# Performance work log

Measured on AMD Instinct MI355X. Metric: run time of the kernel, lower is better.

## Reference

```python
import jax, jax.numpy as jnp
import numpy as np

EMBED = 1024
HEADS = 16
HEAD_DIM = EMBED // HEADS


def setup_inputs() -> dict:
    key = jax.random.key(0)
    ks = jax.random.split(key, 8)
    N, L = 2, 2048
    s = 0.02
    return {
        "values": jax.random.normal(ks[0], (N, L, EMBED), jnp.float32),
        "keys": jax.random.normal(ks[1], (N, L, EMBED), jnp.float32),
        "queries": jax.random.normal(ks[2], (N, L, EMBED), jnp.float32),
        # per-head projection weights, SHARED across heads (nn.Linear(head_dim, head_dim))
        "Wv": jax.random.normal(ks[3], (HEAD_DIM, HEAD_DIM), jnp.float32) * s,
        "Wk": jax.random.normal(ks[4], (HEAD_DIM, HEAD_DIM), jnp.float32) * s,
        "Wq": jax.random.normal(ks[5], (HEAD_DIM, HEAD_DIM), jnp.float32) * s,
        "Wo": jax.random.normal(ks[6], (EMBED, EMBED), jnp.float32) * s,
        "bo": jax.random.normal(ks[7], (EMBED,), jnp.float32) * s,
    }


def reference(values, keys, queries, Wv, Wk, Wq, Wo, bo):
    N, Lq, _ = queries.shape
    Lk = keys.shape[1]
    Lv = values.shape[1]
    # split heads: (N, L, H, D)
    v = values.reshape(N, Lv, HEADS, HEAD_DIM)
    k = keys.reshape(N, Lk, HEADS, HEAD_DIM)
    q = queries.reshape(N, Lq, HEADS, HEAD_DIM)
    # per-head linear (weight shared across heads); nn.Linear computes x @ W.T
    v = jnp.einsum('nlhd,ed->nlhe', v, Wv)
    k = jnp.einsum('nlhd,ed->nlhe', k, Wk)
    q = jnp.einsum('nlhd,ed->nlhe', q, Wq)
    # scores (N, H, Lq, Lk); NOTE: scale uses sqrt(embed_size), as in the original
    scores = jnp.einsum('nqhd,nkhd->nhqk', q, k) / jnp.sqrt(jnp.float32(EMBED))
    attn = jax.nn.softmax(scores, axis=-1)
    out = jnp.einsum('nhql,nlhd->nqhd', attn, v).reshape(N, Lq, EMBED)
    out = out @ Wo.T + bo
    return out
```

## Files before the change

### kernel.cpp

```cpp
#include <hip/hip_runtime.h>
#include <hip/hip_bf16.h>

#define EMBED 1024
#define HEADS 16
#define HD 64
#define NB 2
#define LSEQ 2048

typedef __bf16 bf16x8 __attribute__((ext_vector_type(8)));
typedef float f32x4 __attribute__((ext_vector_type(4)));

static __device__ __forceinline__ __bf16 f2b(float x) {
    union { __hip_bfloat16 h; __bf16 b; } u;
    u.h = __float2bfloat16(x);
    return u.b;
}
static __device__ __forceinline__ bf16x8 cvt8(float4 a, float4 b) {
    bf16x8 r;
    r[0] = f2b(a.x); r[1] = f2b(a.y); r[2] = f2b(a.z); r[3] = f2b(a.w);
    r[4] = f2b(b.x); r[5] = f2b(b.y); r[6] = f2b(b.z); r[7] = f2b(b.w);
    return r;
}
static __device__ __forceinline__ unsigned short b2u(float x) {
    union { __hip_bfloat16 h; unsigned short u; } c;
    c.h = __float2bfloat16(x);
    return c.u;
}

#define GLD16(g, l) __builtin_amdgcn_global_load_lds( \
    (const __attribute__((address_space(1))) void*)(g), \
    (__attribute__((address_space(3))) void*)(l), 16, 0, 0)


__global__ __launch_bounds__(256) void proj_kernel(
    const float* __restrict__ vals,
    const float* __restrict__ keys,
    const float* __restrict__ quer,
    const float* __restrict__ Wv,
    const float* __restrict__ Wk,
    const float* __restrict__ Wq,
    __hip_bfloat16* __restrict__ QF,
    __hip_bfloat16* __restrict__ KF,
    __hip_bfloat16* __restrict__ VF)
{
    int b      = blockIdx.x;
    int tensor = b % 3;
    int rem    = b / 3;
    int n      = rem >> 7;
    int lt     = (rem >> 2) & 31;
    int hg     = rem & 3;
    int t = threadIdx.x, w = t >> 6, lane = t & 63;
    int m16 = lane & 15, quad = lane >> 4;
    int l0 = lt * 64 + w * 16;

    const float* X = (tensor == 0) ? quer : (tensor == 1 ? keys : vals);
    const float* W = (tensor == 0) ? Wq   : (tensor == 1 ? Wk   : Wv);
    float scale = (tensor == 0) ? (1.44269504088896340736f / 32.0f) : 1.0f;

    bf16x8 wf[4][2];
#pragma unroll
    for (int f = 0; f < 4; ++f)
#pragma unroll
        for (int kk = 0; kk < 2; ++kk) {
            const float* wp = W + (f * 16 + m16) * HD + kk * 32 + quad * 8;
            wf[f][kk] = cvt8(*(const float4*)wp, *(const float4*)(wp + 4));
        }

#pragma unroll
    for (int hh = 0; hh < 4; ++hh) {
        int h = hg * 4 + hh;
        const float* xb = X + ((size_t)n * LSEQ + l0 + m16) * EMBED + h * HD + quad * 8;
        bf16x8 xf[2];
#pragma unroll
        for (int kk = 0; kk < 2; ++kk)
            xf[kk] = cvt8(*(const float4*)(xb + kk * 32), *(const float4*)(xb + kk * 32 + 4));

        size_t nhb = (size_t)(n * HEADS + h) * 131072;
        if (tensor != 2) {
            f32x4 acc[4] = {};
#pragma unroll
            for (int f = 0; f < 4; ++f) {
                acc[f] = __builtin_amdgcn_mfma_f32_16x16x32_bf16(wf[f][0], xf[0], acc[f], 0, 0, 0);
                acc[f] = __builtin_amdgcn_mfma_f32_16x16x32_bf16(wf[f][1], xf[1], acc[f], 0, 0, 0);
            }
            int key = l0 + m16;
#pragma unroll
            for (int f = 0; f < 4; ++f) {
                union { ushort4 u; unsigned short s[4]; } p;
#pragma unroll
                for (int r = 0; r < 4; ++r) p.s[r] = b2u(acc[f][r] * scale);
                int kk   = f >> 1;
                int qk2  = (f & 1) * 2 + (quad >> 1);
                int j4   = (quad & 1) * 4;
                __hip_bfloat16* dst;
                if (tensor == 0) {
                    dst = QF + nhb + (size_t)(l0 >> 4) * 1024 + kk * 512
                        + (qk2 * 16 + m16) * 8 + j4;
                } else {
                    dst = KF + nhb + (size_t)(key >> 5) * 2048
                        + ((key & 1) * 2 + kk) * 512
                        + (qk2 * 16 + ((key & 31) >> 1)) * 8 + j4;
                }
                *(ushort4*)dst = p.u;
            }
        } else {
            f32x4 acc[4] = {};
#pragma unroll
            for (int f = 0; f < 4; ++f) {
                acc[f] = __builtin_amdgcn_mfma_f32_16x16x32_bf16(xf[0], wf[f][0], acc[f], 0, 0, 0);
                acc[f] = __builtin_amdgcn_mfma_f32_16x16x32_bf16(xf[1], wf[f][1], acc[f], 0, 0, 0);
            }
            int keyq  = l0 + quad * 4;
            int c     = keyq >> 5;
            int quadv = (keyq & 31) >> 3;
            int j4    = (quad & 1) * 4;
#pragma unroll
            for (int f = 0; f < 4; ++f) {
                union { ushort4 u; unsigned short s[4]; } p;
#pragma unroll
                for (int r = 0; r < 4; ++r) p.s[r] = b2u(acc[f][r]);
                __hip_bfloat16* dst = VF + nhb + (size_t)c * 2048 + f * 512
                    + quadv * 128 + m16 * 8 + j4;
                *(ushort4*)dst = p.u;
            }
        }
    }
}

__global__ __launch_bounds__(256) void wcvt_kernel(
    const float* __restrict__ Wo, __hip_bfloat16* __restrict__ Wob)
{
    int base = (blockIdx.x * 256 + threadIdx.x) * 16;
#pragma unroll
    for (int j = 0; j < 16; j += 4) {
        float4 w4 = *(const float4*)(Wo + base + j);
        __hip_bfloat16 o[4] = {
            __float2bfloat16(w4.x), __float2bfloat16(w4.y),
            __float2bfloat16(w4.z), __float2bfloat16(w4.w)};
        *(ushort4*)(Wob + base + j) = *(const ushort4*)o;
    }
}

#define CHUNKS 32

#define LOADK(KFR, c_) do { \
    const __hip_bfloat16* kc_ = kp + (size_t)(c_) * 2048; \
    KFR[0][0] = *(const bf16x8*)(kc_); \
    KFR[0][1] = *(const bf16x8*)(kc_ + 512); \
    KFR[1][0] = *(const bf16x8*)(kc_ + 1024); \
    KFR[1][1] = *(const bf16x8*)(kc_ + 1536); \
} while (0)

#define LOADV(c_) do { \
    const __hip_bfloat16* vc_ = vp + (size_t)(c_) * 2048; \
    vf[0] = *(const bf16x8*)(vc_); \
    vf[1] = *(const bf16x8*)(vc_ + 512); \
    vf[2] = *(const bf16x8*)(vc_ + 1024); \
    vf[3] = *(const bf16x8*)(vc_ + 1536); \
} while (0)

#define SCORE(KFR, BUF) do { \
    f32x4 s_[2][2]; \
    __builtin_amdgcn_s_setprio(1); \
    _Pragma("unroll") \
    for (int tq_ = 0; tq_ < 2; ++tq_) { \
        _Pragma("unroll") \
        for (int t2_ = 0; t2_ < 2; ++t2_) { \
            f32x4 z_ = {}; \
            z_ = __builtin_amdgcn_mfma_f32_16x16x32_bf16(qf[tq_][0], KFR[t2_][0], z_, 0, 0, 0); \
            z_ = __builtin_amdgcn_mfma_f32_16x16x32_bf16(qf[tq_][1], KFR[t2_][1], z_, 0, 0, 0); \
            s_[tq_][t2_] = z_; \
        } \
    } \
    __builtin_amdgcn_s_setprio(0); \
    _Pragma("unroll") \
    for (int tq_ = 0; tq_ < 2; ++tq_) { \
        _Pragma("unroll") \
        for (int r_ = 0; r_ < 4; ++r_) { \
            float e0_ = __builtin_amdgcn_exp2f(s_[tq_][0][r_]); \
            float e1_ = __builtin_amdgcn_exp2f(s_[tq_][1][r_]); \
            unsigned u_ = __builtin_amdgcn_perm( \
                __float_as_uint(e1_), __float_as_uint(e0_), 0x07060302); \
            *(unsigned*)&Pb[BUF][w][tq_ * 16 + quad * 4 + r_][2 * m16] = u_; \
        } \
    } \
} while (0)

#define PVSTEP(BUF) do { \
    bf16x8 pf0_ = *(const bf16x8*)&Pb[BUF][w][m16][quad * 8]; \
    bf16x8 pf1_ = *(const bf16x8*)&Pb[BUF][w][16 + m16][quad * 8]; \
    __builtin_amdgcn_s_setprio(1); \
    _Pragma("unroll") \
    for (int f_ = 0; f_ < 4; ++f_) { \
        of[0][f_] = __builtin_amdgcn_mfma_f32_16x16x32_bf16(pf0_, vf[f_], of[0][f_], 0, 0, 0); \
        of[1][f_] = __builtin_amdgcn_mfma_f32_16x16x32_bf16(pf1_, vf[f_], of[1][f_], 0, 0, 0); \
    } \
    lsa[0] = __builtin_amdgcn_mfma_f32_16x16x32_bf16(pf0_, onesf, lsa[0], 0, 0, 0); \
    lsa[1] = __builtin_amdgcn_mfma_f32_16x16x32_bf16(pf1_, onesf, lsa[1], 0, 0, 0); \
    __builtin_amdgcn_s_setprio(0); \
} while (0)

__global__ __launch_bounds__(256) void attn_kernel(
    const __hip_bfloat16* __restrict__ QF,
    const __hip_bfloat16* __restrict__ KF,
    const __hip_bfloat16* __restrict__ VF,
    __hip_bfloat16* __restrict__ AO)
{
    __shared__ __align__(16) __hip_bfloat16 Pb[2][4][32][40];

    int i  = blockIdx.x;
    int x  = i & 7, r2 = i >> 3;
    int nh = x * 4 + (r2 >> 5);
    int qblk = r2 & 31;

    int t = threadIdx.x, w = t >> 6, lane = t & 63;
    int m16 = lane & 15, quad = lane >> 4;
    int qh = w & 1, kh = w >> 1;
    int q0 = qblk * 64 + qh * 32;
    size_t nhb = (size_t)nh * 131072;

    const __hip_bfloat16* qb = QF + nhb + (size_t)(q0 >> 4) * 1024 + lane * 8;
    bf16x8 qf[2][2];
#pragma unroll
    for (int tq = 0; tq < 2; ++tq)
#pragma unroll
        for (int kk = 0; kk < 2; ++kk)
            qf[tq][kk] = *(const bf16x8*)(qb + tq * 1024 + kk * 512);

    const __hip_bfloat16* kp = KF + nhb + (size_t)(kh * 32) * 2048 + lane * 8;
    const __hip_bfloat16* vp = VF + nhb + (size_t)(kh * 32) * 2048 + lane * 8;

    bf16x8 onesf;
#pragma unroll
    for (int j = 0; j < 8; ++j) onesf[j] = f2b(1.0f);

    f32x4 of[2][4] = {};
    f32x4 lsa[2] = {};
    bf16x8 kfa[2][2], kfb[2][2], vf[4];

    LOADK(kfa, 0);
    LOADK(kfb, 1);
    SCORE(kfa, 0);
    LOADV(0);

#pragma unroll 1
    for (int tt = 0; tt < 15; ++tt) {
        int c = 2 * tt;
        LOADK(kfa, c + 2);
        SCORE(kfb, 1);
        PVSTEP(0);
        LOADV(c + 1);
        LOADK(kfb, c + 3);
        SCORE(kfa, 0);
        PVSTEP(1);
        LOADV(c + 2);
    }
    SCORE(kfb, 1);
    PVSTEP(0);
    LOADV(31);
    PVSTEP(1);

    __syncthreads();
    float* Cb = (float*)&Pb[0][0][0][0];
    if (kh == 1) {
        int base = qh * 2560;
#pragma unroll
        for (int tq = 0; tq < 2; ++tq)
#pragma unroll
            for (int f = 0; f < 4; ++f)
                *(f32x4*)&Cb[base + (tq * 4 + f) * 256 + lane * 4] = of[tq][f];
#pragma unroll
        for (int tq = 0; tq < 2; ++tq)
#pragma unroll
            for (int r = 0; r < 4; ++r)
                Cb[base + 2048 + (tq * 4 + r) * 64 + lane] = lsa[tq][r];
    }
    __syncthreads();
    if (kh == 0) {
        int base = qh * 2560;
#pragma unroll
        for (int tq = 0; tq < 2; ++tq)
#pragma unroll
            for (int f = 0; f < 4; ++f)
                of[tq][f] += *(const f32x4*)&Cb[base + (tq * 4 + f) * 256 + lane * 4];
        int n = nh >> 4, h = nh & 15;
#pragma unroll
        for (int tq = 0; tq < 2; ++tq)
#pragma unroll
            for (int r = 0; r < 4; ++r) {
                float lt2 = lsa[tq][r] + Cb[base + 2048 + (tq * 4 + r) * 64 + lane];
                float rinv = 1.0f / lt2;
                int qrow = q0 + tq * 16 + quad * 4 + r;
#pragma unroll
                for (int f = 0; f < 4; ++f) {
                    int col = h * HD + f * 16 + m16;
                    AO[((size_t)n * LSEQ + qrow) * EMBED + col] =
                        __float2bfloat16(of[tq][f][r] * rinv);
                }
            }
    }
}

__global__ __launch_bounds__(256) void outproj_kernel(
    const __hip_bfloat16* __restrict__ AO,
    const __hip_bfloat16* __restrict__ Wob,
    const float* __restrict__ bo,
    float* __restrict__ out)
{
    __shared__ __align__(16) __hip_bfloat16 As[128 * 32];
    __shared__ __align__(16) __hip_bfloat16 Bs[64 * 32];

    int b  = blockIdx.x;
    int mt = b >> 4, nt = b & 15;
    int m0 = mt * 128, n0 = nt * 64;
    int t = threadIdx.x, w = t >> 6, lane = t & 63;
    int m16 = lane & 15, quad = lane >> 4;

    int srow = lane >> 2;
    int scol = (lane & 3) * 8;

    const __hip_bfloat16* Ab = AO  + (size_t)m0 * EMBED;
    const __hip_bfloat16* Bb = Wob + (size_t)n0 * EMBED;

    f32x4 acc[2][4] = {};
    for (int k0 = 0; k0 < EMBED; k0 += 32) {
        __syncthreads();
#pragma unroll
        for (int j = 0; j < 2; ++j) {
            int g = j * 4 + w;
            GLD16(Ab + (size_t)(g * 16 + srow) * EMBED + k0 + scol, &As[g * 512]);
        }
        GLD16(Bb + (size_t)(w * 16 + srow) * EMBED + k0 + scol, &Bs[w * 512]);
        __syncthreads();

        bf16x8 af[2], bfr[4];
#pragma unroll
        for (int ta = 0; ta < 2; ++ta)
            af[ta] = *(const bf16x8*)&As[(w * 32 + ta * 16 + m16) * 32 + quad * 8];
#pragma unroll
        for (int tb = 0; tb < 4; ++tb)
            bfr[tb] = *(const bf16x8*)&Bs[(tb * 16 + m16) * 32 + quad * 8];
#pragma unroll
        for (int ta = 0; ta < 2; ++ta)
#pragma unroll
            for (int tb = 0; tb < 4; ++tb)
                acc[ta][tb] = __builtin_amdgcn_mfma_f32_16x16x32_bf16(
                    af[ta], bfr[tb], acc[ta][tb], 0, 0, 0);
    }

#pragma unroll
    for (int tb = 0; tb < 4; ++tb) {
        int col = n0 + tb * 16 + m16;
        float bias = bo[col];
#pragma unroll
        for (int ta = 0; ta < 2; ++ta)
#pragma unroll
            for (int r = 0; r < 4; ++r) {
                int row = m0 + w * 32 + ta * 16 + quad * 4 + r;
                out[(size_t)row * EMBED + col] = acc[ta][tb][r] + bias;
            }
    }
}

extern "C" void kernel_launch(void* const* d_in, const int* in_sizes, int n_in,
                              void* d_out, int out_size, void* d_ws, size_t ws_size,
                              hipStream_t stream) {
    const float* vals = (const float*)d_in[0];
    const float* keys = (const float*)d_in[1];
    const float* quer = (const float*)d_in[2];
    const float* Wv   = (const float*)d_in[3];
    const float* Wk   = (const float*)d_in[4];
    const float* Wq   = (const float*)d_in[5];
    const float* Wo   = (const float*)d_in[6];
    const float* bo   = (const float*)d_in[7];
    float* out = (float*)d_out;

    __hip_bfloat16* ws = (__hip_bfloat16*)d_ws;
    const size_t PE = (size_t)NB * HEADS * LSEQ * HD;
    __hip_bfloat16* QF  = ws;
    __hip_bfloat16* KF  = ws + PE;
    __hip_bfloat16* VF  = ws + 2 * PE;
    __hip_bfloat16* AO  = ws + 3 * PE;
    __hip_bfloat16* Wob = ws + 4 * PE;

    proj_kernel<<<3 * NB * (LSEQ / 64) * (HEADS / 4), 256, 0, stream>>>(
        vals, keys, quer, Wv, Wk, Wq, QF, KF, VF);
    wcvt_kernel<<<256, 256, 0, stream>>>(Wo, Wob);
    attn_kernel<<<1024, 256, 0, stream>>>(QF, KF, VF, AO);
    outproj_kernel<<<512, 256, 0, stream>>>(AO, Wob, bo, out);
}
```

Before: 176.2 us.

## Split projection per head and shrink out-projection M tile for more blocks

The projection kernel now handles one head per block instead of four, which quadruples the grid to expose more parallelism and lowers per-block serial work. The output projection moves from 128x64 to 64x64 tiles with a K step of 64, doubling the grid to 1024 blocks. The trade-off is that each block reloads weights more often, and the smaller out-projection tiles lower reuse of the Wo tile.

```diff
diff --git a/kernel.cpp b/kernel.cpp
--- a/kernel.cpp
+++ b/kernel.cpp
@@ -46,9 +46,9 @@
     int b      = blockIdx.x;
     int tensor = b % 3;
     int rem    = b / 3;
-    int n      = rem >> 7;
-    int lt     = (rem >> 2) & 31;
-    int hg     = rem & 3;
+    int n      = rem >> 9;
+    int lt     = (rem >> 4) & 31;
+    int h      = rem & 15;
     int t = threadIdx.x, w = t >> 6, lane = t & 63;
     int m16 = lane & 15, quad = lane >> 4;
     int l0 = lt * 64 + w * 16;
@@ -57,6 +57,12 @@
     const float* W = (tensor == 0) ? Wq   : (tensor == 1 ? Wk   : Wv);
     float scale = (tensor == 0) ? (1.44269504088896340736f / 32.0f) : 1.0f;
 
+    const float* xb = X + ((size_t)n * LSEQ + l0 + m16) * EMBED + h * HD + quad * 8;
+    bf16x8 xf[2];
+#pragma unroll
+    for (int kk = 0; kk < 2; ++kk)
+        xf[kk] = cvt8(*(const float4*)(xb + kk * 32), *(const float4*)(xb + kk * 32 + 4));
+
     bf16x8 wf[4][2];
 #pragma unroll
     for (int f = 0; f < 4; ++f)
@@ -66,63 +72,53 @@
             wf[f][kk] = cvt8(*(const float4*)wp, *(const float4*)(wp + 4));
         }
 
-#pragma unroll
-    for (int hh = 0; hh < 4; ++hh) {
-        int h = hg * 4 + hh;
-        const float* xb = X + ((size_t)n * LSEQ + l0 + m16) * EMBED + h * HD + quad * 8;
-        bf16x8 xf[2];
-#pragma unroll
-        for (int kk = 0; kk < 2; ++kk)
-            xf[kk] = cvt8(*(const float4*)(xb + kk * 32), *(const float4*)(xb + kk * 32 + 4));
-
-        size_t nhb = (size_t)(n * HEADS + h) * 131072;
-        if (tensor != 2) {
-            f32x4 acc[4] = {};
-#pragma unroll
-            for (int f = 0; f < 4; ++f) {
-                acc[f] = __builtin_amdgcn_mfma_f32_16x16x32_bf16(wf[f][0], xf[0], acc[f], 0, 0, 0);
-                acc[f] = __builtin_amdgcn_mfma_f32_16x16x32_bf16(wf[f][1], xf[1], acc[f], 0, 0, 0);
+    size_t nhb = (size_t)(n * HEADS + h) * 131072;
+    if (tensor != 2) {
+        f32x4 acc[4] = {};
+#pragma unroll
+        for (int f = 0; f < 4; ++f) {
+            acc[f] = __builtin_amdgcn_mfma_f32_16x16x32_bf16(wf[f][0], xf[0], acc[f], 0, 0, 0);
+            acc[f] = __builtin_amdgcn_mfma_f32_16x16x32_bf16(wf[f][1], xf[1], acc[f], 0, 0, 0);
+        }
+        int key = l0 + m16;
+#pragma unroll
+        for (int f = 0; f < 4; ++f) {
+            union { ushort4 u; unsigned short s[4]; } p;
+#pragma unroll
+            for (int r = 0; r < 4; ++r) p.s[r] = b2u(acc[f][r] * scale);
+            int kk   = f >> 1;
+            int qk2  = (f & 1) * 2 + (quad >> 1);
+            int j4   = (quad & 1) * 4;
+            __hip_bfloat16* dst;
+            if (tensor == 0) {
+                dst = QF + nhb + (size_t)(l0 >> 4) * 1024 + kk * 512
+                    + (qk2 * 16 + m16) * 8 + j4;
+            } else {
+                dst = KF + nhb + (size_t)(key >> 5) * 2048
+                    + ((key & 1) * 2 + kk) * 512
+                    + (qk2 * 16 + ((key & 31) >> 1)) * 8 + j4;
             }
-            int key = l0 + m16;
-#pragma unroll
-            for (int f = 0; f < 4; ++f) {
-                union { ushort4 u; unsigned short s[4]; } p;
-#pragma unroll
-                for (int r = 0; r < 4; ++r) p.s[r] = b2u(acc[f][r] * scale);
-                int kk   = f >> 1;
-                int qk2  = (f & 1) * 2 + (quad >> 1);
-                int j4   = (quad & 1) * 4;
-                __hip_bfloat16* dst;
-                if (tensor == 0) {
-                    dst = QF + nhb + (size_t)(l0 >> 4) * 1024 + kk * 512
-                        + (qk2 * 16 + m16) * 8 + j4;
-                } else {
-                    dst = KF + nhb + (size_t)(key >> 5) * 2048
-                        + ((key & 1) * 2 + kk) * 512
-                        + (qk2 * 16 + ((key & 31) >> 1)) * 8 + j4;
-                }
-                *(ushort4*)dst = p.u;
-            }
-        } else {
-            f32x4 acc[4] = {};
-#pragma unroll
-            for (int f = 0; f < 4; ++f) {
-                acc[f] = __builtin_amdgcn_mfma_f32_16x16x32_bf16(xf[0], wf[f][0], acc[f], 0, 0, 0);
-                acc[f] = __builtin_amdgcn_mfma_f32_16x16x32_bf16(xf[1], wf[f][1], acc[f], 0, 0, 0);
-            }
-            int keyq  = l0 + quad * 4;
-            int c     = keyq >> 5;
-            int quadv = (keyq & 31) >> 3;
-            int j4    = (quad & 1) * 4;
-#pragma unroll
-            for (int f = 0; f < 4; ++f) {
-                union { ushort4 u; unsigned short s[4]; } p;
-#pragma unroll
-                for (int r = 0; r < 4; ++r) p.s[r] = b2u(acc[f][r]);
-                __hip_bfloat16* dst = VF + nhb + (size_t)c * 2048 + f * 512
-                    + quadv * 128 + m16 * 8 + j4;
-                *(ushort4*)dst = p.u;
-            }
+            *(ushort4*)dst = p.u;
+        }
+    } else {
+        f32x4 acc[4] = {};
+#pragma unroll
+        for (int f = 0; f < 4; ++f) {
+            acc[f] = __builtin_amdgcn_mfma_f32_16x16x32_bf16(xf[0], wf[f][0], acc[f], 0, 0, 0);
+            acc[f] = __builtin_amdgcn_mfma_f32_16x16x32_bf16(xf[1], wf[f][1], acc[f], 0, 0, 0);
+        }
+        int keyq  = l0 + quad * 4;
+        int c     = keyq >> 5;
+        int quadv = (keyq & 31) >> 3;
+        int j4    = (quad & 1) * 4;
+#pragma unroll
+        for (int f = 0; f < 4; ++f) {
+            union { ushort4 u; unsigned short s[4]; } p;
+#pragma unroll
+            for (int r = 0; r < 4; ++r) p.s[r] = b2u(acc[f][r]);
+            __hip_bfloat16* dst = VF + nhb + (size_t)c * 2048 + f * 512
+                + quadv * 128 + m16 * 8 + j4;
+            *(ushort4*)dst = p.u;
         }
     }
 }
@@ -307,12 +303,12 @@
     const float* __restrict__ bo,
     float* __restrict__ out)
 {
-    __shared__ __align__(16) __hip_bfloat16 As[128 * 32];
-    __shared__ __align__(16) __hip_bfloat16 Bs[64 * 32];
+    __shared__ __align__(16) __hip_bfloat16 As[2][64][32];
+    __shared__ __align__(16) __hip_bfloat16 Bs[2][64][32];
 
     int b  = blockIdx.x;
     int mt = b >> 4, nt = b & 15;
-    int m0 = mt * 128, n0 = nt * 64;
+    int m0 = mt * 64, n0 = nt * 64;
     int t = threadIdx.x, w = t >> 6, lane = t & 63;
     int m16 = lane & 15, quad = lane >> 4;
 
@@ -322,30 +318,29 @@
     const __hip_bfloat16* Ab = AO  + (size_t)m0 * EMBED;
     const __hip_bfloat16* Bb = Wob + (size_t)n0 * EMBED;
 
-    f32x4 acc[2][4] = {};
-    for (int k0 = 0; k0 < EMBED; k0 += 32) {
+    f32x4 acc[4] = {};
+    for (int k0 = 0; k0 < EMBED; k0 += 64) {
         __syncthreads();
-#pragma unroll
-        for (int j = 0; j < 2; ++j) {
-            int g = j * 4 + w;
-            GLD16(Ab + (size_t)(g * 16 + srow) * EMBED + k0 + scol, &As[g * 512]);
-        }
-        GLD16(Bb + (size_t)(w * 16 + srow) * EMBED + k0 + scol, &Bs[w * 512]);
+        GLD16(Ab + (size_t)(w * 16 + srow) * EMBED + k0 +      scol, &As[0][w * 16][0]);
+        GLD16(Ab + (size_t)(w * 16 + srow) * EMBED + k0 + 32 + scol, &As[1][w * 16][0]);
+        GLD16(Bb + (size_t)(w * 16 + srow) * EMBED + k0 +      scol, &Bs[0][w * 16][0]);
+        GLD16(Bb + (size_t)(w * 16 + srow) * EMBED + k0 + 32 + scol, &Bs[1][w * 16][0]);
         __syncthreads();
 
-        bf16x8 af[2], bfr[4];
-#pragma unroll
-        for (int ta = 0; ta < 2; ++ta)
-            af[ta] = *(const bf16x8*)&As[(w * 32 + ta * 16 + m16) * 32 + quad * 8];
-#pragma unroll
-        for (int tb = 0; tb < 4; ++tb)
-            bfr[tb] = *(const bf16x8*)&Bs[(tb * 16 + m16) * 32 + quad * 8];
-#pragma unroll
-        for (int ta = 0; ta < 2; ++ta)
+        bf16x8 af[2], bfr[2][4];
+#pragma unroll
+        for (int kk = 0; kk < 2; ++kk)
+            af[kk] = *(const bf16x8*)&As[kk][w * 16 + m16][quad * 8];
+#pragma unroll
+        for (int kk = 0; kk < 2; ++kk)
 #pragma unroll
             for (int tb = 0; tb < 4; ++tb)
-                acc[ta][tb] = __builtin_amdgcn_mfma_f32_16x16x32_bf16(
-                    af[ta], bfr[tb], acc[ta][tb], 0, 0, 0);
+                bfr[kk][tb] = *(const bf16x8*)&Bs[kk][tb * 16 + m16][quad * 8];
+#pragma unroll
+        for (int tb = 0; tb < 4; ++tb) {
+            acc[tb] = __builtin_amdgcn_mfma_f32_16x16x32_bf16(af[0], bfr[0][tb], acc[tb], 0, 0, 0);
+            acc[tb] = __builtin_amdgcn_mfma_f32_16x16x32_bf16(af[1], bfr[1][tb], acc[tb], 0, 0, 0);
+        }
     }
 
 #pragma unroll
@@ -353,12 +348,10 @@
         int col = n0 + tb * 16 + m16;
         float bias = bo[col];
 #pragma unroll
-        for (int ta = 0; ta < 2; ++ta)
-#pragma unroll
-            for (int r = 0; r < 4; ++r) {
-                int row = m0 + w * 32 + ta * 16 + quad * 4 + r;
-                out[(size_t)row * EMBED + col] = acc[ta][tb][r] + bias;
-            }
+        for (int r = 0; r < 4; ++r) {
+            int row = m0 + w * 16 + quad * 4 + r;
+            out[(size_t)row * EMBED + col] = acc[tb][r] + bias;
+        }
     }
 }
 
@@ -383,9 +376,9 @@
     __hip_bfloat16* AO  = ws + 3 * PE;
     __hip_bfloat16* Wob = ws + 4 * PE;
 
-    proj_kernel<<<3 * NB * (LSEQ / 64) * (HEADS / 4), 256, 0, stream>>>(
+    proj_kernel<<<3 * NB * (LSEQ / 64) * HEADS, 256, 0, stream>>>(
         vals, keys, quer, Wv, Wk, Wq, QF, KF, VF);
     wcvt_kernel<<<256, 256, 0, stream>>>(Wo, Wob);
     attn_kernel<<<1024, 256, 0, stream>>>(QF, KF, VF, AO);
-    outproj_kernel<<<512, 256, 0, stream>>>(AO, Wob, bo, out);
-}
+    outproj_kernel<<<1024, 256, 0, stream>>>(AO, Wob, bo, out);
+}
```

Measured after the change: 182.3 us. 3.5% more time.
